# Performance work log

Hardware: AMD Instinct MI355X
Metric: run time of the kernel (lower is better)

## Reference

```python
import jax, jax.numpy as jnp
import numpy as np
import math

N = 20000          # nodes (residues)
E = 640000         # edges
CS = 384           # c_s
CZ = 128           # c_z
CH = 16            # c_hidden
H = 8              # no_heads
PQK = 8            # no_qk_points == no_v_points (forced equal, see notes)
FS = 128           # scalar channels in feat_irreps
PIN = 16           # vector channels in feat_irreps
HC = H * CH        # 128
HPQ = H * PQK * 3  # 192
CZ4 = CZ // 4      # 32
OUT_IN = HC + 3 * H + H + H * CZ4  # 416 actual concat width
INF = 100000.0
EPS = 1e-8


def setup_inputs() -> dict:
    key = jax.random.key(0)
    ks = jax.random.split(key, 16)
    w = lambda k, i, o: (jax.random.normal(k, (i, o), jnp.float32) / np.float32(np.sqrt(i)))
    frame_s = jax.random.normal(ks[0], (N, CS), jnp.float32)
    tfn_t = jax.random.normal(ks[1], (N, FS + 3 * PIN), jnp.float32)
    z = jax.random.normal(ks[2], (E, CZ), jnp.float32)
    edge_index = jax.random.randint(ks[3], (2, E), 0, N)
    mask = jnp.ones((N,), jnp.float32)
    # Rigid transforms: proper-ish rotations via QR, translations
    rot, _ = jnp.linalg.qr(jax.random.normal(ks[4], (N, 3, 3), jnp.float32))
    trans = jax.random.normal(ks[5], (N, 3), jnp.float32)
    return {
        "frame_s": frame_s, "tfn_t": tfn_t, "z": z,
        "edge_index": edge_index, "mask": mask,
        "rot": rot, "trans": trans,
        "Wq": w(ks[6], CS, HC), "bq": jnp.zeros((HC,), jnp.float32),
        "Wk_s": w(ks[7], FS, HC), "Wk_v": w(ks[8], PIN, PQK),
        "Wqp": w(ks[9], CS, HPQ), "bqp": jnp.zeros((HPQ,), jnp.float32),
        "Wb": w(ks[10], CZ, H), "bb": jnp.zeros((H,), jnp.float32),
        "Wdz": w(ks[11], CZ, CZ4), "bdz": jnp.zeros((CZ4,), jnp.float32),
        # ipa_point_weights_init_: softplus(hw) == 1  =>  hw = log(e - 1)
        "head_weights": jnp.full((H,), np.float32(np.log(np.e - 1.0))),
        "Wout": w(ks[12], OUT_IN, CS), "bout": jnp.zeros((CS,), jnp.float32),
    }


def _segment_softmax(a, seg, n):
    # pyg-style numerically stable segment softmax over edges grouped by seg
    m = jax.ops.segment_max(a, seg, num_segments=n)
    m = jnp.where(jnp.isfinite(m), m, 0.0)
    e = jnp.exp(a - m[seg])
    s = jax.ops.segment_sum(e, seg, num_segments=n)
    return e / (s[seg] + 1e-16)


def _forward(frame_s, tfn_t, z, mask, rot, trans,
             Wq, bq, Wk_s, Wk_v, Wqp, bqp, Wb, bb, Wdz, bdz,
             head_weights, Wout, bout, edge_index):
    n = frame_s.shape[0]
    src = edge_index[1]
    dst = edge_index[0]

    # scalar queries: [N,H,C]
    q = (frame_s @ Wq + bq).reshape(n, H, CH)

    # o3.Linear (feat_irreps -> k_irreps): scalars mix scalars, vectors mix vectors.
    # NOTE: original code uses linear_k for BOTH k and v (faithful bug), so v==k.
    scal = tfn_t[:, :FS]
    vecs = tfn_t[:, FS:].reshape(n, PIN, 3)
    k_scal = scal @ Wk_s                                   # [N, HC]
    k_vec = jnp.einsum('npx,pq->nqx', vecs, Wk_v)          # [N, PQK, 3]
    k = k_scal.reshape(n, H, CH)
    v = k
    k_tail = k_vec.reshape(n, PQK * 3)                     # [N, 24]
    # torch: split([3]*PQK) then stack(dim=-1) -> [N,3,PQK], then view [N,H,-1,3]
    k_pts = jnp.stack(jnp.split(k_tail, PQK, axis=-1), axis=-1)  # [N,3,PQK]
    k_pts = k_pts.reshape(n, H, -1, 3)                     # [N,H,1,3]
    v_pts = k_pts

    # query points, rigid-transformed: [N,H,PQK,3]
    q_pts = frame_s @ Wqp + bqp                            # [N, 3*H*PQK]
    q_pts = jnp.stack(jnp.split(q_pts, 3, axis=-1), axis=-1)  # [N, H*PQK, 3]
    q_pts = jnp.einsum('nij,npj->npi', rot, q_pts) + trans[:, None, :]
    q_pts = q_pts.reshape(n, H, PQK, 3)

    # scalar attention logits [E,H]
    a = jnp.einsum('ehc,ehc->eh', q[src], k[dst])
    a = a * np.float32(math.sqrt(1.0 / (3 * CH)))
    b = z @ Wb + bb                                        # [E,H]
    a = a + np.float32(math.sqrt(1.0 / 3)) * b

    # point attention: disp [E,H,PQK,3] (k_pts broadcasts over points)
    disp = q_pts[src] - k_pts[dst]
    pt_att = jnp.sum(disp * disp, axis=-1)                 # [E,H,PQK]
    hw = jax.nn.softplus(head_weights) * np.float32(math.sqrt(1.0 / (3 * (PQK * 9.0 / 2))))
    pt_att = -0.5 * jnp.sum(pt_att * hw[None, :, None], axis=-1)  # [E,H]

    edge_mask = INF * (mask[dst] * mask[src] - 1.0)        # [E]
    a = a + pt_att + edge_mask[:, None]

    a = _segment_softmax(a, src, n)                        # [E,H]

    # scalar output
    o = jax.ops.segment_sum(a[..., None] * v[dst], src, num_segments=n)  # [N,H,C]
    o = o.reshape(n, HC)

    # point output
    o_pt = jax.ops.segment_sum(a[:, :, None, None] * v_pts[dst], src, num_segments=n)  # [N,H,1,3]
    o_pt = jnp.einsum('nji,nhpj->nhpi', rot, o_pt - trans[:, None, None, :])  # invert_apply
    o_pt_norm = jnp.sqrt(jnp.sum(o_pt * o_pt, axis=-1) + EPS).reshape(n, H)
    o_pt = o_pt.reshape(n, -1, 3)                          # [N,H,3]

    # pair output
    pair_z = z @ Wdz + bdz                                 # [E,CZ4]
    o_pair = jax.ops.segment_sum(a[..., None] * pair_z[:, None, :], src, num_segments=n)  # [N,H,CZ4]
    o_pair = o_pair.reshape(n, H * CZ4)

    feats = jnp.concatenate(
        [o, o_pt[..., 0], o_pt[..., 1], o_pt[..., 2], o_pt_norm, o_pair], axis=-1)  # [N,416]
    return feats @ Wout + bout                             # [N, CS]


def reference(frame_s, tfn_t, z, edge_index, mask, rot, trans,
              Wq, bq, Wk_s, Wk_v, Wqp, bqp, Wb, bb, Wdz, bdz,
              head_weights, Wout, bout):
    return _forward(frame_s, tfn_t, z, mask, rot, trans,
                    Wq, bq, Wk_s, Wk_v, Wqp, bqp, Wb, bb, Wdz, bdz,
                    head_weights, Wout, bout, edge_index)
```

## Files before the change

### kernel.cpp

```cpp
#include <hip/hip_runtime.h>
#include <math.h>

typedef __attribute__((ext_vector_type(8))) short short8;
typedef __attribute__((ext_vector_type(4))) float f32x4;

static __device__ inline unsigned short f2bf(float f) {
    union { float f; unsigned u; } v; v.f = f;
    unsigned r = v.u + 0x7FFF + ((v.u >> 16) & 1);
    return (unsigned short)(r >> 16);
}

template<int WJ>
__device__ __forceinline__ void gemm_body(
    unsigned short* __restrict__ As, unsigned short* __restrict__ Bs,
    const float* __restrict__ A, int lda,
    const float* __restrict__ BT, int ldb,
    const float* __restrict__ bias,
    float* __restrict__ C, int ldc,
    int M, int N, int K, int bx, int by)
{
    constexpr int GBN = WJ * 32;
    const int t = threadIdx.x;
    const int wid = t >> 6, lane = t & 63;
    const int wm = (wid & 1) * 64;
    const int wn = (wid >> 1) * (WJ * 16);
    const int row16 = lane & 15, quad = lane >> 4;
    const int bm = bx * 128;
    const int bn = by * GBN;

    f32x4 acc[4][WJ];
    #pragma unroll
    for (int i = 0; i < 4; ++i)
        #pragma unroll
        for (int j = 0; j < WJ; ++j)
            #pragma unroll
            for (int r = 0; r < 4; ++r) acc[i][j][r] = 0.f;

    const int ktiles = (K + 63) >> 6;
    for (int kt = 0; kt < ktiles; ++kt) {
        const int k0 = kt << 6;
        #pragma unroll
        for (int it = 0; it < 8; ++it) {
            int f = it * 256 + t;
            int row = f >> 4, kq = (f & 15) << 2;
            float4 av = make_float4(0.f, 0.f, 0.f, 0.f);
            if (bm + row < M && k0 + kq < K)
                av = *(const float4*)(A + (size_t)(bm + row) * lda + k0 + kq);
            ushort4 uv;
            uv.x = f2bf(av.x); uv.y = f2bf(av.y); uv.z = f2bf(av.z); uv.w = f2bf(av.w);
            *(ushort4*)(&As[row * 72 + kq]) = uv;
        }
        #pragma unroll
        for (int it = 0; it < WJ * 2; ++it) {
            int f = it * 256 + t;
            int row = f >> 4, kq = (f & 15) << 2;
            float4 bv = make_float4(0.f, 0.f, 0.f, 0.f);
            if (bn + row < N && k0 + kq < K)
                bv = *(const float4*)(BT + (size_t)(bn + row) * ldb + k0 + kq);
            ushort4 uv;
            uv.x = f2bf(bv.x); uv.y = f2bf(bv.y); uv.z = f2bf(bv.z); uv.w = f2bf(bv.w);
            *(ushort4*)(&Bs[row * 72 + kq]) = uv;
        }
        __syncthreads();

        #pragma unroll
        for (int ks = 0; ks < 64; ks += 32) {
            short8 af[4], bfv[WJ];
            #pragma unroll
            for (int i = 0; i < 4; ++i)
                af[i] = *(const short8*)(&As[(wm + i * 16 + row16) * 72 + ks + quad * 8]);
            #pragma unroll
            for (int j = 0; j < WJ; ++j)
                bfv[j] = *(const short8*)(&Bs[(wn + j * 16 + row16) * 72 + ks + quad * 8]);
            #pragma unroll
            for (int i = 0; i < 4; ++i)
                #pragma unroll
                for (int j = 0; j < WJ; ++j)
                    acc[i][j] = __builtin_amdgcn_mfma_f32_16x16x32_bf16(af[i], bfv[j], acc[i][j], 0, 0, 0);
        }
        __syncthreads();
    }

    #pragma unroll
    for (int i = 0; i < 4; ++i)
        #pragma unroll
        for (int j = 0; j < WJ; ++j) {
            int col = bn + wn + j * 16 + row16;
            if (col >= N) continue;
            float bv = bias ? bias[col] : 0.f;
            #pragma unroll
            for (int r = 0; r < 4; ++r) {
                int row = bm + wm + i * 16 + quad * 4 + r;
                if (row < M) C[(size_t)row * ldc + col] = acc[i][j][r] + bv;
            }
        }
}

template<int WJ>
__global__ __launch_bounds__(256) void gemm_mfma(
    const float* __restrict__ A, int lda,
    const float* __restrict__ BT, int ldb,
    const float* __restrict__ bias,
    float* __restrict__ C, int ldc,
    int M, int N, int K)
{
    __shared__ unsigned short As[128 * 72];
    __shared__ unsigned short Bs[WJ * 32 * 72];
    gemm_body<WJ>(As, Bs, A, lda, BT, ldb, bias, C, ldc, M, N, K, blockIdx.x, blockIdx.y);
}

__global__ __launch_bounds__(256) void mega_kernel(
    const float* __restrict__ z, const float* __restrict__ wcatT,
    const float* __restrict__ bcat, float* __restrict__ bpair, int E,
    const float* __restrict__ frame_s, const float* __restrict__ wqqpT,
    const float* __restrict__ bqqp, float* __restrict__ qqp, int n,
    const float* __restrict__ tfn, const float* __restrict__ wksT,
    float* __restrict__ kbuf,
    const float* __restrict__ Wkv, float* __restrict__ kpts,
    const int* __restrict__ srcA, int* __restrict__ cur, int* __restrict__ elist,
    int nb_bp, int nb_qqp_x, int nb_qqp, int nb_k, int nb_kpts)
{
    __shared__ unsigned short As[128 * 72];
    __shared__ unsigned short Bs[128 * 72];
    int b = blockIdx.x;
    if (b < nb_bp) {
        gemm_body<2>(As, Bs, z, 128, wcatT, 128, bcat, bpair, 40, E, 40, 128, b, 0);
        return;
    }
    b -= nb_bp;
    if (b < nb_qqp) {
        gemm_body<4>(As, Bs, frame_s, 384, wqqpT, 384, bqqp, qqp, 320, n, 320, 384,
                     b % nb_qqp_x, b / nb_qqp_x);
        return;
    }
    b -= nb_qqp;
    if (b < nb_k) {
        gemm_body<4>(As, Bs, tfn, 176, wksT, 128, nullptr, kbuf, 128, n, 128, 128, b, 0);
        return;
    }
    b -= nb_k;
    if (b < nb_kpts) {
        int t = b * 256 + threadIdx.x;
        if (t < n * 24) {
            int node = t / 24, f = t % 24;
            int a = f >> 3;
            int bb2 = f & 7;
            const float* vr = tfn + (size_t)node * 176 + 128;
            float s = 0.f;
            #pragma unroll
            for (int p = 0; p < 16; ++p) s += vr[p * 3 + a] * Wkv[p * 8 + bb2];
            kpts[t] = s;
        }
        return;
    }
    b -= nb_kpts;
    {
        int e = b * 256 + threadIdx.x;
        if (e < E) {
            int s = srcA[e];
            int pos = atomicAdd(&cur[s], 1);
            elist[pos] = e;
        }
    }
}

__global__ void prep_kernel(const float* __restrict__ Wq, const float* __restrict__ bq,
                            const float* __restrict__ Wqp, const float* __restrict__ bqp,
                            const float* __restrict__ Wb, const float* __restrict__ bb,
                            const float* __restrict__ Wdz, const float* __restrict__ bdz,
                            const float* __restrict__ Wks, const float* __restrict__ Wout,
                            float* __restrict__ wqqpT, float* __restrict__ bqqp,
                            float* __restrict__ wcatT, float* __restrict__ bcat,
                            float* __restrict__ wksT, float* __restrict__ woutT,
                            int* __restrict__ cnt, int n)
{
    const float SC_QK = 0.14433756729740643f;
    const float SC_B  = 0.5773502691896258f;
    int gid = blockIdx.x * 256 + threadIdx.x;
    int stride = gridDim.x * 256;
    for (int i = gid; i < n; i += stride) cnt[i] = 0;
    for (int i = gid; i < 320 * 384; i += stride) {
        int o = i / 384, c = i % 384;
        wqqpT[i] = (o < 128) ? Wq[c * 128 + o] * SC_QK : Wqp[c * 192 + (o - 128)];
    }
    for (int i = gid; i < 320; i += stride) bqqp[i] = (i < 128) ? bq[i] * SC_QK : bqp[i - 128];
    for (int i = gid; i < 40 * 128; i += stride) {
        int o = i >> 7, c = i & 127;
        wcatT[i] = (o < 8) ? Wb[c * 8 + o] * SC_B : Wdz[c * 32 + (o - 8)];
    }
    for (int i = gid; i < 40; i += stride) bcat[i] = (i < 8) ? bb[i] * SC_B : bdz[i - 8];
    for (int i = gid; i < 128 * 128; i += stride) {
        int o = i >> 7, c = i & 127;
        wksT[i] = Wks[c * 128 + o];
    }
    for (int i = gid; i < 384 * 416; i += stride) {
        int o = i / 416, c = i % 416;
        woutT[i] = Wout[c * 384 + o];
    }
}

__global__ void count_kernel(const int* __restrict__ srcA, int* __restrict__ cnt, int E)
{
    int e = blockIdx.x * 256 + threadIdx.x;
    if (e < E) atomicAdd(&cnt[srcA[e]], 1);
}

__global__ void scan_kernel(const int* __restrict__ cnt, int* __restrict__ off,
                            int* __restrict__ cur, int n)
{
    __shared__ int sums[1024];
    int t = threadIdx.x;
    int chunk = (n + 1023) >> 10;
    int begin = t * chunk;
    int local = 0;
    for (int j = 0; j < chunk; ++j) {
        int i = begin + j;
        if (i < n) local += cnt[i];
    }
    sums[t] = local;
    __syncthreads();
    for (int d = 1; d < 1024; d <<= 1) {
        int x = sums[t];
        int y = (t >= d) ? sums[t - d] : 0;
        __syncthreads();
        sums[t] = x + y;
        __syncthreads();
    }
    int run = sums[t] - local;
    for (int j = 0; j < chunk; ++j) {
        int i = begin + j;
        if (i < n) {
            off[i] = run;
            cur[i] = run;
            run += cnt[i];
        }
    }
}

__global__ __launch_bounds__(256) void attn_kernel(
    const int* __restrict__ off, const int* __restrict__ cnt,
    const int* __restrict__ elist, const int* __restrict__ dstA,
    const float* __restrict__ qqp, const float* __restrict__ kbuf,
    const float* __restrict__ kpts,
    const float* __restrict__ bpair, const float* __restrict__ mask,
    const float* __restrict__ hwin,
    const float* __restrict__ rot, const float* __restrict__ trans,
    float* __restrict__ feats, int n)
{
    int wave = threadIdx.x >> 6;
    int lane = threadIdx.x & 63;
    int s = blockIdx.x * 4 + wave;
    if (s >= n) return;
    int es = lane >> 3;
    int h  = lane & 7;

    float qh[16];
    {
        const float* qp = qqp + (size_t)s * 320 + h * 16;
        #pragma unroll
        for (int c = 0; c < 16; ++c) qh[c] = qp[c];
    }
    const float* Rp = rot + (size_t)s * 9;
    const float* Tp = trans + (size_t)s * 3;
    float R0 = Rp[0], R1 = Rp[1], R2 = Rp[2];
    float R3 = Rp[3], R4 = Rp[4], R5 = Rp[5];
    float R6 = Rp[6], R7 = Rp[7], R8 = Rp[8];
    float T0 = Tp[0], T1 = Tp[1], T2 = Tp[2];
    float qpt[24];
    {
        const float* qr = qqp + (size_t)s * 320 + 128 + h * 8;
        #pragma unroll
        for (int p2 = 0; p2 < 8; ++p2) {
            float c0 = qr[p2], c1 = qr[64 + p2], c2 = qr[128 + p2];
            qpt[p2 * 3 + 0] = R0 * c0 + R1 * c1 + R2 * c2 + T0;
            qpt[p2 * 3 + 1] = R3 * c0 + R4 * c1 + R5 * c2 + T1;
            qpt[p2 * 3 + 2] = R6 * c0 + R7 * c1 + R8 * c2 + T2;
        }
    }
    float hwv = log1pf(__expf(hwin[h])) * 0.04811252243246882f;
    float mask_s = mask[s];
    int myoff = off[s], mycnt = cnt[s];

    float ssum = 0.f;
    float oacc[16];
    #pragma unroll
    for (int c = 0; c < 16; ++c) oacc[c] = 0.f;
    float optacc[3] = {0.f, 0.f, 0.f};
    float opacc[8][4];
    #pragma unroll
    for (int j = 0; j < 8; ++j)
        #pragma unroll
        for (int c = 0; c < 4; ++c) opacc[j][c] = 0.f;

    int nb = (mycnt + 7) >> 3;
    for (int b = 0; b < nb; ++b) {
        int idx = b * 8 + es;
        bool valid = idx < mycnt;
        int e = valid ? elist[myoff + idx] : 0;
        int d = dstA[e];

        const float* kr = kbuf + (size_t)d * 128 + h * 16;
        float4 ka = *(const float4*)(kr + 0);
        float4 kb = *(const float4*)(kr + 4);
        float4 kc = *(const float4*)(kr + 8);
        float4 kd = *(const float4*)(kr + 12);

        const float* kp = kpts + (size_t)d * 24 + h * 3;
        float kp0 = kp[0], kp1 = kp[1], kp2 = kp[2];

        const float* bp = bpair + (size_t)e * 40;
        float bh = bp[h];
        float4 pair4 = *(const float4*)(bp + 8 + h * 4);

        float qk = qh[0] * ka.x + qh[1] * ka.y + qh[2] * ka.z + qh[3] * ka.w
                 + qh[4] * kb.x + qh[5] * kb.y + qh[6] * kb.z + qh[7] * kb.w
                 + qh[8] * kc.x + qh[9] * kc.y + qh[10] * kc.z + qh[11] * kc.w
                 + qh[12] * kd.x + qh[13] * kd.y + qh[14] * kd.z + qh[15] * kd.w;

        float pt = 0.f;
        #pragma unroll
        for (int pp = 0; pp < 8; ++pp) {
            float d0 = qpt[pp * 3 + 0] - kp0;
            float d1 = qpt[pp * 3 + 1] - kp1;
            float d2 = qpt[pp * 3 + 2] - kp2;
            pt += d0 * d0 + d1 * d1 + d2 * d2;
        }

        float md = mask[d];
        float logit = qk + bh - hwv * pt + 100000.0f * (mask_s * md - 1.0f);
        float w = valid ? __expf(logit) : 0.f;

        ssum += w;
        oacc[0] += w * ka.x; oacc[1] += w * ka.y; oacc[2] += w * ka.z; oacc[3] += w * ka.w;
        oacc[4] += w * kb.x; oacc[5] += w * kb.y; oacc[6] += w * kb.z; oacc[7] += w * kb.w;
        oacc[8] += w * kc.x; oacc[9] += w * kc.y; oacc[10] += w * kc.z; oacc[11] += w * kc.w;
        oacc[12] += w * kd.x; oacc[13] += w * kd.y; oacc[14] += w * kd.z; oacc[15] += w * kd.w;
        optacc[0] += w * kp0;
        optacc[1] += w * kp1;
        optacc[2] += w * kp2;

        #pragma unroll
        for (int jh = 0; jh < 8; ++jh) {
            float wj = __shfl(w, (es << 3) + jh);
            opacc[jh][0] += wj * pair4.x;
            opacc[jh][1] += wj * pair4.y;
            opacc[jh][2] += wj * pair4.z;
            opacc[jh][3] += wj * pair4.w;
        }
    }

    #pragma unroll
    for (int delta = 8; delta <= 32; delta <<= 1) {
        ssum += __shfl_xor(ssum, delta);
        #pragma unroll
        for (int c = 0; c < 16; ++c) oacc[c] += __shfl_xor(oacc[c], delta);
        #pragma unroll
        for (int i = 0; i < 3; ++i) optacc[i] += __shfl_xor(optacc[i], delta);
        #pragma unroll
        for (int j = 0; j < 8; ++j)
            #pragma unroll
            for (int c = 0; c < 4; ++c) opacc[j][c] += __shfl_xor(opacc[j][c], delta);
    }

    float invj[8];
    #pragma unroll
    for (int jh = 0; jh < 8; ++jh)
        invj[jh] = 1.f / (__shfl(ssum, jh) + 1e-16f);

    if (es == 0) {
        float inv = 1.f / (ssum + 1e-16f);
        float* f = feats + (size_t)s * 416;
        #pragma unroll
        for (int c = 0; c < 16; c += 4) {
            float4 v = make_float4(oacc[c] * inv, oacc[c + 1] * inv, oacc[c + 2] * inv, oacc[c + 3] * inv);
            *(float4*)(&f[h * 16 + c]) = v;
        }
        float v0 = optacc[0] * inv - T0;
        float v1 = optacc[1] * inv - T1;
        float v2 = optacc[2] * inv - T2;
        float r0 = R0 * v0 + R3 * v1 + R6 * v2;
        float r1 = R1 * v0 + R4 * v1 + R7 * v2;
        float r2 = R2 * v0 + R5 * v1 + R8 * v2;
        f[128 + h] = r0;
        f[136 + h] = r1;
        f[144 + h] = r2;
        f[152 + h] = sqrtf(r0 * r0 + r1 * r1 + r2 * r2 + 1e-8f);
        #pragma unroll
        for (int jh = 0; jh < 8; ++jh) {
            float4 v = make_float4(opacc[jh][0] * invj[jh], opacc[jh][1] * invj[jh],
                                   opacc[jh][2] * invj[jh], opacc[jh][3] * invj[jh]);
            *(float4*)(&f[160 + jh * 32 + h * 4]) = v;
        }
    }
}

extern "C" void kernel_launch(void* const* d_in, const int* in_sizes, int n_in,
                              void* d_out, int out_size, void* d_ws, size_t ws_size,
                              hipStream_t stream)
{
    const float* frame_s = (const float*)d_in[0];
    const float* tfn     = (const float*)d_in[1];
    const float* z       = (const float*)d_in[2];
    const int*   ei      = (const int*)d_in[3];
    const float* mask    = (const float*)d_in[4];
    const float* rot     = (const float*)d_in[5];
    const float* trans   = (const float*)d_in[6];
    const float* Wq      = (const float*)d_in[7];
    const float* bq      = (const float*)d_in[8];
    const float* Wks     = (const float*)d_in[9];
    const float* Wkv     = (const float*)d_in[10];
    const float* Wqp     = (const float*)d_in[11];
    const float* bqp     = (const float*)d_in[12];
    const float* Wb      = (const float*)d_in[13];
    const float* bb      = (const float*)d_in[14];
    const float* Wdz     = (const float*)d_in[15];
    const float* bdz     = (const float*)d_in[16];
    const float* hw      = (const float*)d_in[17];
    const float* Wout    = (const float*)d_in[18];
    const float* bout    = (const float*)d_in[19];
    float* out = (float*)d_out;

    int n = in_sizes[0] / 384;
    int E = in_sizes[3] / 2;
    const int* dstA = ei;
    const int* srcA = ei + E;

    float* ws = (float*)d_ws;
    size_t p = 0;
    auto alloc = [&](size_t elems) -> float* {
        float* r = ws + p;
        p += (elems + 15) & ~((size_t)15);
        return r;
    };
    float* qqpbuf = alloc((size_t)n * 320);
    float* kbuf   = alloc((size_t)n * 128);
    float* kpts   = alloc((size_t)n * 24);
    float* feats  = alloc((size_t)n * 416);
    float* bpair  = alloc((size_t)E * 40);
    float* wqqpT  = alloc(320 * 384);
    float* bqqp   = alloc(320);
    float* wcatT  = alloc(40 * 128);
    float* bcat   = alloc(64);
    float* wksT   = alloc(128 * 128);
    float* woutT  = alloc(384 * 416);
    int* cnt   = (int*)alloc((size_t)n);
    int* off   = (int*)alloc((size_t)n);
    int* cur   = (int*)alloc((size_t)n);
    int* elist = (int*)alloc((size_t)E);

    prep_kernel<<<512, 256, 0, stream>>>(Wq, bq, Wqp, bqp, Wb, bb, Wdz, bdz, Wks, Wout,
                                         wqqpT, bqqp, wcatT, bcat, wksT, woutT, cnt, n);

    count_kernel<<<(E + 255) / 256, 256, 0, stream>>>(srcA, cnt, E);
    scan_kernel<<<1, 1024, 0, stream>>>(cnt, off, cur, n);

    int nb_bp    = (E + 127) / 128;
    int nb_qqp_x = (n + 127) / 128;
    int nb_qqp   = nb_qqp_x * 3;
    int nb_k     = (n + 127) / 128;
    int nb_kpts  = (n * 24 + 255) / 256;
    int nb_fill  = (E + 255) / 256;
    int nb_total = nb_bp + nb_qqp + nb_k + nb_kpts + nb_fill;
    mega_kernel<<<nb_total, 256, 0, stream>>>(
        z, wcatT, bcat, bpair, E,
        frame_s, wqqpT, bqqp, qqpbuf, n,
        tfn, wksT, kbuf,
        Wkv, kpts,
        srcA, cur, elist,
        nb_bp, nb_qqp_x, nb_qqp, nb_k, nb_kpts);

    attn_kernel<<<(n + 3) / 4, 256, 0, stream>>>(off, cnt, elist, dstA,
                                                 qqpbuf, kbuf, kpts, bpair, mask, hw,
                                                 rot, trans, feats, n);

    {
        dim3 g((n + 127) / 128, 3);
        gemm_mfma<4><<<g, 256, 0, stream>>>(feats, 416, woutT, 416, bout, out, 384, n, 384, 416);
    }
    (void)n_in; (void)out_size; (void)ws_size;
}
```

Measured before the change: 914.2 us.

## Split edge pair-bias GEMM into register-resident streaming MFMA kernel

Moves the z @ [Wb|Wdz] edge projection out of the tiled LDS GEMM in the mega kernel into a dedicated persistent kernel. That kernel keeps the small 40x128 weight in registers as bf16 fragments and streams 32-row strips of z directly from global memory into MFMA. The goal is to stop wasting a 64-wide N tile and LDS staging on a 40-column output, so this memory-bound pass runs closer to bandwidth. It adds a separate launch and gives up overlap with the node GEMMs that used to share the mega kernel.

```diff
diff --git a/kernel.cpp b/kernel.cpp
--- a/kernel.cpp
+++ b/kernel.cpp
@@ -109,25 +109,110 @@
     gemm_body<WJ>(As, Bs, A, lda, BT, ldb, bias, C, ldc, M, N, K, blockIdx.x, blockIdx.y);
 }
 
+__global__ __launch_bounds__(256) void bpair_stream(
+    const float* __restrict__ z, const float* __restrict__ wcatT,
+    const float* __restrict__ bcat, float* __restrict__ bpair, int E)
+{
+    const int lane = threadIdx.x & 63;
+    const int wid = threadIdx.x >> 6;
+    const int row16 = lane & 15, quad = lane >> 4;
+
+    short8 bfv[3][4];
+    float bj[3];
+    #pragma unroll
+    for (int j = 0; j < 3; ++j) {
+        int col = j * 16 + row16;
+        bool cv = col < 40;
+        bj[j] = cv ? bcat[col] : 0.f;
+        #pragma unroll
+        for (int ks = 0; ks < 4; ++ks) {
+            float4 w0 = make_float4(0.f, 0.f, 0.f, 0.f);
+            float4 w1 = make_float4(0.f, 0.f, 0.f, 0.f);
+            if (cv) {
+                const float* wp = wcatT + (size_t)col * 128 + ks * 32 + quad * 8;
+                w0 = *(const float4*)(wp);
+                w1 = *(const float4*)(wp + 4);
+            }
+            short8 f;
+            f[0] = (short)f2bf(w0.x); f[1] = (short)f2bf(w0.y);
+            f[2] = (short)f2bf(w0.z); f[3] = (short)f2bf(w0.w);
+            f[4] = (short)f2bf(w1.x); f[5] = (short)f2bf(w1.y);
+            f[6] = (short)f2bf(w1.z); f[7] = (short)f2bf(w1.w);
+            bfv[j][ks] = f;
+        }
+    }
+
+    const int nstrips = (E + 31) >> 5;
+    const int gw = blockIdx.x * 4 + wid;
+    const int nw = gridDim.x * 4;
+    for (int st = gw; st < nstrips; st += nw) {
+        const int r0 = st * 32;
+        short8 af[2][4];
+        #pragma unroll
+        for (int i = 0; i < 2; ++i) {
+            int row = r0 + i * 16 + row16;
+            bool rv = row < E;
+            const float* zp = z + (size_t)row * 128 + quad * 8;
+            #pragma unroll
+            for (int ks = 0; ks < 4; ++ks) {
+                float4 a0 = make_float4(0.f, 0.f, 0.f, 0.f);
+                float4 a1 = make_float4(0.f, 0.f, 0.f, 0.f);
+                if (rv) {
+                    a0 = *(const float4*)(zp + ks * 32);
+                    a1 = *(const float4*)(zp + ks * 32 + 4);
+                }
+                short8 f;
+                f[0] = (short)f2bf(a0.x); f[1] = (short)f2bf(a0.y);
+                f[2] = (short)f2bf(a0.z); f[3] = (short)f2bf(a0.w);
+                f[4] = (short)f2bf(a1.x); f[5] = (short)f2bf(a1.y);
+                f[6] = (short)f2bf(a1.z); f[7] = (short)f2bf(a1.w);
+                af[i][ks] = f;
+            }
+        }
+
+        f32x4 acc[2][3];
+        #pragma unroll
+        for (int i = 0; i < 2; ++i)
+            #pragma unroll
+            for (int j = 0; j < 3; ++j)
+                #pragma unroll
+                for (int r = 0; r < 4; ++r) acc[i][j][r] = 0.f;
+
+        #pragma unroll
+        for (int ks = 0; ks < 4; ++ks)
+            #pragma unroll
+            for (int i = 0; i < 2; ++i)
+                #pragma unroll
+                for (int j = 0; j < 3; ++j)
+                    acc[i][j] = __builtin_amdgcn_mfma_f32_16x16x32_bf16(af[i][ks], bfv[j][ks], acc[i][j], 0, 0, 0);
+
+        #pragma unroll
+        for (int i = 0; i < 2; ++i)
+            #pragma unroll
+            for (int j = 0; j < 3; ++j) {
+                int col = j * 16 + row16;
+                if (col >= 40) continue;
+                #pragma unroll
+                for (int r = 0; r < 4; ++r) {
+                    int row = r0 + i * 16 + quad * 4 + r;
+                    if (row < E) bpair[(size_t)row * 40 + col] = acc[i][j][r] + bj[j];
+                }
+            }
+    }
+}
+
 __global__ __launch_bounds__(256) void mega_kernel(
-    const float* __restrict__ z, const float* __restrict__ wcatT,
-    const float* __restrict__ bcat, float* __restrict__ bpair, int E,
     const float* __restrict__ frame_s, const float* __restrict__ wqqpT,
     const float* __restrict__ bqqp, float* __restrict__ qqp, int n,
     const float* __restrict__ tfn, const float* __restrict__ wksT,
     float* __restrict__ kbuf,
     const float* __restrict__ Wkv, float* __restrict__ kpts,
-    const int* __restrict__ srcA, int* __restrict__ cur, int* __restrict__ elist,
-    int nb_bp, int nb_qqp_x, int nb_qqp, int nb_k, int nb_kpts)
+    const int* __restrict__ srcA, int* __restrict__ cur, int* __restrict__ elist, int E,
+    int nb_qqp_x, int nb_qqp, int nb_k, int nb_kpts)
 {
     __shared__ unsigned short As[128 * 72];
     __shared__ unsigned short Bs[128 * 72];
     int b = blockIdx.x;
-    if (b < nb_bp) {
-        gemm_body<2>(As, Bs, z, 128, wcatT, 128, bcat, bpair, 40, E, 40, 128, b, 0);
-        return;
-    }
-    b -= nb_bp;
     if (b < nb_qqp) {
         gemm_body<4>(As, Bs, frame_s, 384, wqqpT, 384, bqqp, qqp, 320, n, 320, 384,
                      b % nb_qqp_x, b / nb_qqp_x);
@@ -454,20 +539,20 @@
     count_kernel<<<(E + 255) / 256, 256, 0, stream>>>(srcA, cnt, E);
     scan_kernel<<<1, 1024, 0, stream>>>(cnt, off, cur, n);
 
-    int nb_bp    = (E + 127) / 128;
+    bpair_stream<<<2048, 256, 0, stream>>>(z, wcatT, bcat, bpair, E);
+
     int nb_qqp_x = (n + 127) / 128;
     int nb_qqp   = nb_qqp_x * 3;
     int nb_k     = (n + 127) / 128;
     int nb_kpts  = (n * 24 + 255) / 256;
     int nb_fill  = (E + 255) / 256;
-    int nb_total = nb_bp + nb_qqp + nb_k + nb_kpts + nb_fill;
+    int nb_total = nb_qqp + nb_k + nb_kpts + nb_fill;
     mega_kernel<<<nb_total, 256, 0, stream>>>(
-        z, wcatT, bcat, bpair, E,
         frame_s, wqqpT, bqqp, qqpbuf, n,
         tfn, wksT, kbuf,
         Wkv, kpts,
-        srcA, cur, elist,
-        nb_bp, nb_qqp_x, nb_qqp, nb_k, nb_kpts);
+        srcA, cur, elist, E,
+        nb_qqp_x, nb_qqp, nb_k, nb_kpts);
 
     attn_kernel<<<(n + 3) / 4, 256, 0, stream>>>(off, cnt, elist, dstA,
                                                  qqpbuf, kbuf, kpts, bpair, mask, hw,
```

Result: faster. 856.9 us (-6.3%).
